# Kernel tuning notes

Hardware: AMD Instinct MI355X
Metric: run time of the kernel (lower is better)

## Reference

```python
import jax, jax.numpy as jnp
import numpy as np

THRESHOLD = 0.5
NEG_POS_RATIO = 3
ALPHA = 1.0
N_CLASSES = 81
B, P, M = 32, 8732, 16


def cxcy_to_xy(c):
    return jnp.concatenate([c[..., :2] - c[..., 2:] / 2, c[..., :2] + c[..., 2:] / 2], -1)


def xy_to_cxcy(x):
    return jnp.concatenate([(x[..., :2] + x[..., 2:]) / 2, x[..., 2:] - x[..., :2]], -1)


def cxcy_to_gcxgcy(c, p):
    # SSD box encoding with variances 0.1 / 0.2
    return jnp.concatenate([(c[..., :2] - p[..., :2]) / (p[..., 2:] / 10.0),
                            jnp.log(c[..., 2:] / p[..., 2:]) * 5.0], -1)


def box_iou(a, b):
    # a: [M,4], b: [P,4] in xy (xmin,ymin,xmax,ymax)
    lt = jnp.maximum(a[:, None, :2], b[None, :, :2])
    rb = jnp.minimum(a[:, None, 2:], b[None, :, 2:])
    wh = jnp.clip(rb - lt, 0.0)
    inter = wh[..., 0] * wh[..., 1]
    area_a = (a[:, 2] - a[:, 0]) * (a[:, 3] - a[:, 1])
    area_b = (b[:, 2] - b[:, 0]) * (b[:, 3] - b[:, 1])
    return inter / (area_a[:, None] + area_b[None, :] - inter)


def setup_inputs() -> dict:
    key = jax.random.key(0)
    k1, k2, k3, k4, k5, k6, k7 = jax.random.split(key, 7)
    predicted_locs = jax.random.normal(k1, (B, P, 4), dtype=jnp.float32)
    predicted_logits = jax.random.normal(k2, (B, P, N_CLASSES), dtype=jnp.float32)
    # valid gt boxes: centers in (0.2,0.8), sizes in (0.05,0.4) -> xy
    cxy = jax.random.uniform(k3, (B, M, 2), minval=0.2, maxval=0.8)
    wh = jax.random.uniform(k4, (B, M, 2), minval=0.05, maxval=0.4)
    boxes = cxcy_to_xy(jnp.concatenate([cxy, wh], -1)).astype(jnp.float32)
    labels = jax.random.randint(k5, (B, M), 1, N_CLASSES)  # real objects: labels >= 1
    # priors: centers in (0,1), positive sizes
    pcxy = jax.random.uniform(k6, (P, 2), minval=0.0, maxval=1.0)
    pwh = jax.random.uniform(k7, (P, 2), minval=0.05, maxval=0.6)
    priors_cxcy = jnp.concatenate([pcxy, pwh], -1).astype(jnp.float32)
    return {"predicted_locs": predicted_locs, "predicted_logits": predicted_logits,
            "boxes": boxes, "labels": labels, "priors_cxcy": priors_cxcy}


def reference(predicted_locs, predicted_logits, boxes, labels, priors_cxcy):
    priors_xy = cxcy_to_xy(priors_cxcy)

    def match(bx, lb):  # bx: [M,4] xy, lb: [M] int
        overlap = box_iou(bx, priors_xy)                # [M, P]
        overlap_for_each_prior = overlap.max(axis=0)    # [P]
        object_for_each_prior = overlap.argmax(axis=0)  # [P]
        prior_for_each_object = overlap.argmax(axis=1)  # [M]
        # force each gt object to be matched to its best prior
        object_for_each_prior = object_for_each_prior.at[prior_for_each_object].set(jnp.arange(M))
        overlap_for_each_prior = overlap_for_each_prior.at[prior_for_each_object].set(1.0)
        label_for_each_prior = lb[object_for_each_prior]
        label_for_each_prior = jnp.where(overlap_for_each_prior < THRESHOLD, 0, label_for_each_prior)
        true_locs = cxcy_to_gcxgcy(xy_to_cxcy(bx[object_for_each_prior]), priors_cxcy)
        return true_locs, label_for_each_prior

    true_locs, true_classes = jax.vmap(match)(boxes, labels)  # [B,P,4], [B,P]

    positive = true_classes != 0                 # [B,P]
    n_positives = positive.sum(axis=1)           # [B]
    n_pos_total = n_positives.sum().astype(jnp.float32)

    # localization: L1Loss (mean) over positive priors only -> mean over 4*n_pos elements
    loc_loss = jnp.sum(jnp.abs(predicted_locs - true_locs) * positive[..., None]) / (4.0 * n_pos_total)

    # per-prior cross entropy, nan/inf -> 0 as in the original
    logp = jax.nn.log_softmax(predicted_logits, axis=-1)
    conf_loss_all = -jnp.take_along_axis(logp, true_classes[..., None], axis=-1)[..., 0]  # [B,P]
    conf_loss_all = jnp.nan_to_num(conf_loss_all, nan=0.0, posinf=0.0, neginf=0.0)

    conf_loss_pos_sum = jnp.sum(conf_loss_all * positive)
    conf_loss_neg = jnp.where(positive, 0.0, conf_loss_all)
    conf_loss_neg = -jnp.sort(-conf_loss_neg, axis=1)  # descending sort per image
    ranks = jnp.arange(P)[None, :]
    hard_negatives = ranks < (NEG_POS_RATIO * n_positives)[:, None]
    conf_loss_hard_neg_sum = jnp.sum(conf_loss_neg * hard_negatives)

    conf_loss = (conf_loss_hard_neg_sum + conf_loss_pos_sum) / n_pos_total
    return conf_loss + ALPHA * loc_loss
```

## Files before the change

### kernel.cpp

```cpp
#include <hip/hip_runtime.h>
#include <math.h>

#define BB 32
#define PP 8732
#define MM 16
#define NC 81
#define THRESH 0.5f
#define NPR 3
#define CHUNKS 16
#define CHUNK ((PP + CHUNKS - 1) / CHUNKS)
#define SBLK 64

__global__ void __launch_bounds__(256) match_part_kernel(
    const float* __restrict__ boxes,
    const float* __restrict__ priors,
    float* __restrict__ ovl,
    int* __restrict__ obj,
    unsigned long long* __restrict__ keys_part)
{
    const int b = blockIdx.x / CHUNKS;
    const int c = blockIdx.x % CHUNKS;
    const int tid = threadIdx.x;
    __shared__ float s_box[MM][4];
    __shared__ float s_area[MM];
    __shared__ float s_bv[4 * MM];
    __shared__ int   s_bi[4 * MM];

    if (tid < MM * 4) ((float*)s_box)[tid] = boxes[b * MM * 4 + tid];
    __syncthreads();
    if (tid < MM)
        s_area[tid] = (s_box[tid][2] - s_box[tid][0]) * (s_box[tid][3] - s_box[tid][1]);
    __syncthreads();

    float bestv[MM];
    int   bestp[MM];
#pragma unroll
    for (int m = 0; m < MM; ++m) { bestv[m] = -1.0f; bestp[m] = 0; }

    const int p0 = c * CHUNK;
    const int p1 = (p0 + CHUNK < PP) ? (p0 + CHUNK) : PP;
    for (int p = p0 + tid; p < p1; p += 256) {
        const float4 pr = ((const float4*)priors)[p];
        float px0 = pr.x - pr.z * 0.5f, py0 = pr.y - pr.w * 0.5f;
        float px1 = pr.x + pr.z * 0.5f, py1 = pr.y + pr.w * 0.5f;
        float parea = (px1 - px0) * (py1 - py0);
        float bv = -1.0f; int bm = 0;
#pragma unroll
        for (int m = 0; m < MM; ++m) {
            float lx = fmaxf(s_box[m][0], px0);
            float ly = fmaxf(s_box[m][1], py0);
            float rx = fminf(s_box[m][2], px1);
            float ry = fminf(s_box[m][3], py1);
            float w = fmaxf(rx - lx, 0.0f);
            float h = fmaxf(ry - ly, 0.0f);
            float inter = w * h;
            float iou = inter / (s_area[m] + parea - inter);
            if (iou > bv) { bv = iou; bm = m; }
            if (iou > bestv[m]) { bestv[m] = iou; bestp[m] = p; }
        }
        ovl[b * PP + p] = bv;
        obj[b * PP + p] = bm;
    }

    const int lane = tid & 63, wid = tid >> 6;
#pragma unroll
    for (int m = 0; m < MM; ++m) {
        float v = bestv[m]; int i = bestp[m];
        for (int off = 32; off > 0; off >>= 1) {
            float ov = __shfl_xor(v, off);
            int   oi = __shfl_xor(i, off);
            if (ov > v || (ov == v && oi < i)) { v = ov; i = oi; }
        }
        if (lane == 0) { s_bv[wid * MM + m] = v; s_bi[wid * MM + m] = i; }
    }
    __syncthreads();

    if (tid == 0) {
        for (int m = 0; m < MM; ++m) {
            float v = s_bv[m]; int i = s_bi[m];
            for (int w = 1; w < 4; ++w) {
                float ov = s_bv[w * MM + m]; int oi = s_bi[w * MM + m];
                if (ov > v || (ov == v && oi < i)) { v = ov; i = oi; }
            }
            if (v < 0.0f) v = 0.0f;
            keys_part[(b * CHUNKS + c) * MM + m] =
                ((unsigned long long)__float_as_uint(v) << 32) |
                (unsigned long long)(0x7FFFFFFFu - (unsigned)i);
        }
    }
}

__global__ void __launch_bounds__(512) force_match_kernel(
    const unsigned long long* __restrict__ keys_part,
    float* __restrict__ ovl, int* __restrict__ obj)
{
    __shared__ int s_p[BB * MM];
    const int tid = threadIdx.x;
    const int b = tid >> 4, m = tid & 15;

    unsigned long long best = 0ull;
#pragma unroll
    for (int c = 0; c < CHUNKS; ++c) {
        unsigned long long k = keys_part[(b * CHUNKS + c) * MM + m];
        if (k > best) best = k;
    }
    s_p[tid] = (int)(0x7FFFFFFFu - (unsigned)(best & 0xFFFFFFFFull));
    __syncthreads();

    if (m == 0) {
        for (int mm = 0; mm < MM; ++mm) {
            int p = s_p[(b << 4) + mm];
            obj[b * PP + p] = mm;
            ovl[b * PP + p] = 1.0f;
        }
    }
}

__global__ void __launch_bounds__(256) conf_kernel(
    const float* __restrict__ logits,
    const float* __restrict__ plocs,
    const float* __restrict__ boxes,
    const int*   __restrict__ labels,
    const float* __restrict__ priors,
    const float* __restrict__ ovl,
    const int*   __restrict__ obj,
    float* __restrict__ neg,
    int*   __restrict__ cnt_part,
    float* __restrict__ conf_part,
    float* __restrict__ loc_part)
{
    const int tid = threadIdx.x;
    const int lane = tid & 63;
    const int g = lane >> 4;
    const int i = lane & 15;
    const int b = blockIdx.x / SBLK;
    const int s = blockIdx.x % SBLK;
    const int w0 = s * 4 + (tid >> 6);
    const int GPI = PP / 4;

    int   pcnt = 0;
    float pconf = 0.0f, ploc = 0.0f;

    for (int wi = w0; wi < GPI; wi += SBLK * 4) {
        const int rp = wi * 4 + g;
        const int r = b * PP + rp;
        const float ov = ovl[r];
        const int o = obj[r];
        const int lab = labels[b * MM + o];

        const size_t base = (size_t)r * NC;
        float e0 = logits[base + i];
        float e1 = logits[base + 16 + i];
        float e2 = logits[base + 32 + i];
        float e3 = logits[base + 48 + i];
        float e4 = logits[base + 64 + i];
        float e5 = (i == 0) ? logits[base + 80] : -INFINITY;

        float mx = fmaxf(fmaxf(fmaxf(e0, e1), fmaxf(e2, e3)), fmaxf(e4, e5));
#pragma unroll
        for (int off = 8; off > 0; off >>= 1) mx = fmaxf(mx, __shfl_xor(mx, off));
        float sum = __expf(e0 - mx) + __expf(e1 - mx) + __expf(e2 - mx) +
                    __expf(e3 - mx) + __expf(e4 - mx) +
                    ((i == 0) ? __expf(e5 - mx) : 0.0f);
#pragma unroll
        for (int off = 8; off > 0; off >>= 1) sum += __shfl_xor(sum, off);

        const int cls = (ov < THRESH) ? 0 : lab;
        const int k = cls >> 4, ci = cls & 15;
        float ek = (k == 0) ? e0 : (k == 1) ? e1 : (k == 2) ? e2 :
                   (k == 3) ? e3 : (k == 4) ? e4 : e5;
        float xc = __shfl(ek, (g << 4) + ci);
        float conf = mx + __logf(sum) - xc;
        if (!isfinite(conf)) conf = 0.0f;

        if (i == 0) {
            neg[r] = (cls == 0) ? conf : 0.0f;
            if (cls != 0) {
                pcnt += 1;
                pconf += conf;
                const float4 bx = ((const float4*)boxes)[b * MM + o];
                float cx = (bx.x + bx.z) * 0.5f;
                float cy = (bx.y + bx.w) * 0.5f;
                float w4 = bx.z - bx.x;
                float h4 = bx.w - bx.y;
                const float4 pr = ((const float4*)priors)[rp];
                float g0 = (cx - pr.x) / (pr.z / 10.0f);
                float g1 = (cy - pr.y) / (pr.w / 10.0f);
                float g2 = logf(w4 / pr.z) * 5.0f;
                float g3 = logf(h4 / pr.w) * 5.0f;
                const float4 pl = ((const float4*)plocs)[r];
                ploc += fabsf(pl.x - g0) + fabsf(pl.y - g1) +
                        fabsf(pl.z - g2) + fabsf(pl.w - g3);
            }
        }
    }

    __shared__ int   s4i[4];
    __shared__ float s4c[4], s4l[4];
#pragma unroll
    for (int off = 32; off > 0; off >>= 1) {
        pcnt  += __shfl_xor(pcnt, off);
        pconf += __shfl_xor(pconf, off);
        ploc  += __shfl_xor(ploc, off);
    }
    const int wv = tid >> 6;
    if (lane == 0) { s4i[wv] = pcnt; s4c[wv] = pconf; s4l[wv] = ploc; }
    __syncthreads();
    if (tid == 0) {
        cnt_part[blockIdx.x]  = s4i[0] + s4i[1] + s4i[2] + s4i[3];
        conf_part[blockIdx.x] = s4c[0] + s4c[1] + s4c[2] + s4c[3];
        loc_part[blockIdx.x]  = s4l[0] + s4l[1] + s4l[2] + s4l[3];
    }
}

#define TPK 1024
#define VPT ((PP + TPK - 1) / TPK)

__global__ void __launch_bounds__(TPK) topk_kernel(
    const float* __restrict__ neg, const int* __restrict__ cnt_part,
    float* __restrict__ hardneg)
{
    const int b = blockIdx.x;
    const int tid = threadIdx.x;
    const int lane = tid & 63, wid = tid >> 6;
    __shared__ int s16i[16];
    __shared__ float s16f[16];
    __shared__ int s_k;

    if (tid < 64) {
        int c = cnt_part[b * SBLK + tid];
#pragma unroll
        for (int off = 32; off > 0; off >>= 1) c += __shfl_xor(c, off);
        if (tid == 0) s_k = NPR * c;
    }

    unsigned v[VPT];
#pragma unroll
    for (int j = 0; j < VPT; ++j) {
        int p = tid + j * TPK;
        v[j] = (p < PP) ? __float_as_uint(neg[b * PP + p]) : 0u;
    }
    __syncthreads();

    int K = s_k;
    if (K > PP) K = PP;
    if (K <= 0) { if (tid == 0) hardneg[b] = 0.0f; return; }

    unsigned lo = 0u, hi = 0x7fffffffu;
    while (lo < hi) {
        unsigned mid = lo + ((hi - lo + 1u) >> 1);
        int cnt = 0;
#pragma unroll
        for (int j = 0; j < VPT; ++j) cnt += (v[j] >= mid);
#pragma unroll
        for (int off = 32; off > 0; off >>= 1) cnt += __shfl_xor(cnt, off);
        if (lane == 0) s16i[wid] = cnt;
        __syncthreads();
        int total = 0;
#pragma unroll
        for (int j = 0; j < 16; ++j) total += s16i[j];
        __syncthreads();
        if (total >= K) lo = mid; else hi = mid - 1u;
    }
    const unsigned kth = lo;

    int cgt = 0; float sgt = 0.0f;
#pragma unroll
    for (int j = 0; j < VPT; ++j) {
        if (v[j] > kth) { cgt++; sgt += __uint_as_float(v[j]); }
    }
#pragma unroll
    for (int off = 32; off > 0; off >>= 1) {
        cgt += __shfl_xor(cgt, off);
        sgt += __shfl_xor(sgt, off);
    }
    if (lane == 0) { s16i[wid] = cgt; s16f[wid] = sgt; }
    __syncthreads();
    if (tid == 0) {
        int cgt_t = 0; float sum_gt = 0.0f;
#pragma unroll
        for (int j = 0; j < 16; ++j) { cgt_t += s16i[j]; sum_gt += s16f[j]; }
        hardneg[b] = sum_gt + (float)(K - cgt_t) * __uint_as_float(kth);
    }
}

__global__ void __launch_bounds__(256) final_kernel(
    const int* __restrict__ cnt_part,
    const float* __restrict__ conf_part,
    const float* __restrict__ loc_part,
    const float* __restrict__ hardneg,
    float* __restrict__ out)
{
    const int tid = threadIdx.x;
    const int lane = tid & 63, wid = tid >> 6;
    __shared__ int s4i[4];
    __shared__ float s4c[4], s4l[4], s4h[4];

    int np = 0; float cf = 0.0f, lc = 0.0f, hn = 0.0f;
    for (int j = tid; j < BB * SBLK; j += 256) {
        np += cnt_part[j];
        cf += conf_part[j];
        lc += loc_part[j];
    }
    if (tid < BB) hn = hardneg[tid];

#pragma unroll
    for (int off = 32; off > 0; off >>= 1) {
        np += __shfl_xor(np, off);
        cf += __shfl_xor(cf, off);
        lc += __shfl_xor(lc, off);
        hn += __shfl_xor(hn, off);
    }
    if (lane == 0) { s4i[wid] = np; s4c[wid] = cf; s4l[wid] = lc; s4h[wid] = hn; }
    __syncthreads();
    if (tid == 0) {
        float npt = (float)(s4i[0] + s4i[1] + s4i[2] + s4i[3]);
        float cft = s4c[0] + s4c[1] + s4c[2] + s4c[3];
        float lct = s4l[0] + s4l[1] + s4l[2] + s4l[3];
        float hnt = s4h[0] + s4h[1] + s4h[2] + s4h[3];
        out[0] = (hnt + cft) / npt + lct / (4.0f * npt);
    }
}

extern "C" void kernel_launch(void* const* d_in, const int* in_sizes, int n_in,
                              void* d_out, int out_size, void* d_ws, size_t ws_size,
                              hipStream_t stream) {
    (void)in_sizes; (void)n_in; (void)out_size; (void)ws_size;
    const float* plocs  = (const float*)d_in[0];
    const float* logits = (const float*)d_in[1];
    const float* boxes  = (const float*)d_in[2];
    const int*   labels = (const int*)d_in[3];
    const float* priors = (const float*)d_in[4];
    float* out = (float*)d_out;

    char* ws = (char*)d_ws;
    float* ovl      = (float*)ws; ws += (size_t)BB * PP * 4;
    int*   obj      = (int*)ws;   ws += (size_t)BB * PP * 4;
    float* neg      = (float*)ws; ws += (size_t)BB * PP * 4;
    unsigned long long* keys_part = (unsigned long long*)ws; ws += (size_t)BB * CHUNKS * MM * 8;
    int*   cnt_part  = (int*)ws;   ws += BB * SBLK * 4;
    float* conf_part = (float*)ws; ws += BB * SBLK * 4;
    float* loc_part  = (float*)ws; ws += BB * SBLK * 4;
    float* hardneg   = (float*)ws; ws += BB * 4;


    match_part_kernel<<<BB * CHUNKS, 256, 0, stream>>>(boxes, priors, ovl, obj, keys_part);
    force_match_kernel<<<1, 512, 0, stream>>>(keys_part, ovl, obj);

    conf_kernel<<<BB * SBLK, 256, 0, stream>>>(logits, plocs, boxes, labels, priors,
                                               ovl, obj, neg,
                                               cnt_part, conf_part, loc_part);

    topk_kernel<<<BB, TPK, 0, stream>>>(neg, cnt_part, hardneg);

    final_kernel<<<1, 256, 0, stream>>>(cnt_part, conf_part, loc_part, hardneg, out);
}
```

Baseline: 75.23 us.

## Recompute per-prior IoU in conf kernel and fuse force-match and final reduction

The match kernel no longer writes per-prior best overlap and object index. It only produces the per-object best-prior keys. The conf kernel recomputes the IoU per prior, with one lane per gt box, takes the argmax with shuffles, and applies the forced matches through a ballot over the reduced keys. The separate force-match and final kernels are removed: the last top-k block, found with an atomic counter, does the global reduction. This cuts two launches and the ovl/obj global round trips, at the cost of redundant IoU math and a fence-based last-block pattern.

Measured after the change: 87.43 us. +16.2%, slower.

```diff
diff --git a/kernel.cpp b/kernel.cpp
--- a/kernel.cpp
+++ b/kernel.cpp
@@ -14,13 +14,14 @@
 __global__ void __launch_bounds__(256) match_part_kernel(
     const float* __restrict__ boxes,
     const float* __restrict__ priors,
-    float* __restrict__ ovl,
-    int* __restrict__ obj,
-    unsigned long long* __restrict__ keys_part)
+    unsigned long long* __restrict__ keys_part,
+    unsigned* __restrict__ done)
 {
     const int b = blockIdx.x / CHUNKS;
     const int c = blockIdx.x % CHUNKS;
     const int tid = threadIdx.x;
+    if (blockIdx.x == 0 && tid == 0) *done = 0u;
+
     __shared__ float s_box[MM][4];
     __shared__ float s_area[MM];
     __shared__ float s_bv[4 * MM];
@@ -44,7 +45,6 @@
         float px0 = pr.x - pr.z * 0.5f, py0 = pr.y - pr.w * 0.5f;
         float px1 = pr.x + pr.z * 0.5f, py1 = pr.y + pr.w * 0.5f;
         float parea = (px1 - px0) * (py1 - py0);
-        float bv = -1.0f; int bm = 0;
 #pragma unroll
         for (int m = 0; m < MM; ++m) {
             float lx = fmaxf(s_box[m][0], px0);
@@ -55,11 +55,8 @@
             float h = fmaxf(ry - ly, 0.0f);
             float inter = w * h;
             float iou = inter / (s_area[m] + parea - inter);
-            if (iou > bv) { bv = iou; bm = m; }
             if (iou > bestv[m]) { bestv[m] = iou; bestp[m] = p; }
         }
-        ovl[b * PP + p] = bv;
-        obj[b * PP + p] = bm;
     }
 
     const int lane = tid & 63, wid = tid >> 6;
@@ -90,40 +87,13 @@
     }
 }
 
-__global__ void __launch_bounds__(512) force_match_kernel(
-    const unsigned long long* __restrict__ keys_part,
-    float* __restrict__ ovl, int* __restrict__ obj)
-{
-    __shared__ int s_p[BB * MM];
-    const int tid = threadIdx.x;
-    const int b = tid >> 4, m = tid & 15;
-
-    unsigned long long best = 0ull;
-#pragma unroll
-    for (int c = 0; c < CHUNKS; ++c) {
-        unsigned long long k = keys_part[(b * CHUNKS + c) * MM + m];
-        if (k > best) best = k;
-    }
-    s_p[tid] = (int)(0x7FFFFFFFu - (unsigned)(best & 0xFFFFFFFFull));
-    __syncthreads();
-
-    if (m == 0) {
-        for (int mm = 0; mm < MM; ++mm) {
-            int p = s_p[(b << 4) + mm];
-            obj[b * PP + p] = mm;
-            ovl[b * PP + p] = 1.0f;
-        }
-    }
-}
-
 __global__ void __launch_bounds__(256) conf_kernel(
     const float* __restrict__ logits,
     const float* __restrict__ plocs,
     const float* __restrict__ boxes,
     const int*   __restrict__ labels,
     const float* __restrict__ priors,
-    const float* __restrict__ ovl,
-    const int*   __restrict__ obj,
+    const unsigned long long* __restrict__ keys_part,
     float* __restrict__ neg,
     int*   __restrict__ cnt_part,
     float* __restrict__ conf_part,
@@ -135,6 +105,34 @@
     const int i = lane & 15;
     const int b = blockIdx.x / SBLK;
     const int s = blockIdx.x % SBLK;
+
+    __shared__ float s_box[MM][4];
+    __shared__ float s_area[MM];
+    __shared__ int   s_lab[MM];
+    __shared__ int   s_fp[MM];
+    __shared__ unsigned long long s_keys[CHUNKS * MM];
+
+    if (tid < MM * 4) ((float*)s_box)[tid] = boxes[b * MM * 4 + tid];
+    if (tid < MM) s_lab[tid] = labels[b * MM + tid];
+    s_keys[tid] = keys_part[b * CHUNKS * MM + tid];
+    __syncthreads();
+    if (tid < MM) {
+        s_area[tid] = (s_box[tid][2] - s_box[tid][0]) * (s_box[tid][3] - s_box[tid][1]);
+        unsigned long long best = 0ull;
+#pragma unroll
+        for (int c = 0; c < CHUNKS; ++c) {
+            unsigned long long k = s_keys[c * MM + tid];
+            if (k > best) best = k;
+        }
+        s_fp[tid] = (int)(0x7FFFFFFFu - (unsigned)(best & 0xFFFFFFFFull));
+    }
+    __syncthreads();
+
+    const float bxx0 = s_box[i][0], bxy0 = s_box[i][1];
+    const float bxx1 = s_box[i][2], bxy1 = s_box[i][3];
+    const float barea = s_area[i];
+    const int   myfp  = s_fp[i];
+
     const int w0 = s * 4 + (tid >> 6);
     const int GPI = PP / 4;
 
@@ -144,9 +142,27 @@
     for (int wi = w0; wi < GPI; wi += SBLK * 4) {
         const int rp = wi * 4 + g;
         const int r = b * PP + rp;
-        const float ov = ovl[r];
-        const int o = obj[r];
-        const int lab = labels[b * MM + o];
+
+        const float4 pr = ((const float4*)priors)[rp];
+        float px0 = pr.x - pr.z * 0.5f, py0 = pr.y - pr.w * 0.5f;
+        float px1 = pr.x + pr.z * 0.5f, py1 = pr.y + pr.w * 0.5f;
+        float parea = (px1 - px0) * (py1 - py0);
+        float lx = fmaxf(bxx0, px0), ly = fmaxf(bxy0, py0);
+        float rx = fminf(bxx1, px1), ry = fminf(bxy1, py1);
+        float inter = fmaxf(rx - lx, 0.0f) * fmaxf(ry - ly, 0.0f);
+        float ov = inter / (barea + parea - inter);
+        int bm = i;
+#pragma unroll
+        for (int off = 8; off > 0; off >>= 1) {
+            float o2 = __shfl_xor(ov, off);
+            int   i2 = __shfl_xor(bm, off);
+            if (o2 > ov || (o2 == ov && i2 < bm)) { ov = o2; bm = i2; }
+        }
+        unsigned long long bal = __ballot(myfp == rp);
+        unsigned gm = (unsigned)((bal >> (g * 16)) & 0xFFFFull);
+        int o, cls;
+        if (gm) { o = 31 - __clz(gm); cls = s_lab[o]; }
+        else    { o = bm; cls = (ov < THRESH) ? 0 : s_lab[bm]; }
 
         const size_t base = (size_t)r * NC;
         float e0 = logits[base + i];
@@ -165,7 +181,6 @@
 #pragma unroll
         for (int off = 8; off > 0; off >>= 1) sum += __shfl_xor(sum, off);
 
-        const int cls = (ov < THRESH) ? 0 : lab;
         const int k = cls >> 4, ci = cls & 15;
         float ek = (k == 0) ? e0 : (k == 1) ? e1 : (k == 2) ? e2 :
                    (k == 3) ? e3 : (k == 4) ? e4 : e5;
@@ -178,12 +193,10 @@
             if (cls != 0) {
                 pcnt += 1;
                 pconf += conf;
-                const float4 bx = ((const float4*)boxes)[b * MM + o];
-                float cx = (bx.x + bx.z) * 0.5f;
-                float cy = (bx.y + bx.w) * 0.5f;
-                float w4 = bx.z - bx.x;
-                float h4 = bx.w - bx.y;
-                const float4 pr = ((const float4*)priors)[rp];
+                float cx = (s_box[o][0] + s_box[o][2]) * 0.5f;
+                float cy = (s_box[o][1] + s_box[o][3]) * 0.5f;
+                float w4 = s_box[o][2] - s_box[o][0];
+                float h4 = s_box[o][3] - s_box[o][1];
                 float g0 = (cx - pr.x) / (pr.z / 10.0f);
                 float g1 = (cy - pr.y) / (pr.w / 10.0f);
                 float g2 = logf(w4 / pr.z) * 5.0f;
@@ -216,9 +229,11 @@
 #define TPK 1024
 #define VPT ((PP + TPK - 1) / TPK)
 
-__global__ void __launch_bounds__(TPK) topk_kernel(
+__global__ void __launch_bounds__(TPK) topk_final_kernel(
     const float* __restrict__ neg, const int* __restrict__ cnt_part,
-    float* __restrict__ hardneg)
+    const float* __restrict__ conf_part, const float* __restrict__ loc_part,
+    float* __restrict__ hardneg, unsigned* __restrict__ done,
+    float* __restrict__ out)
 {
     const int b = blockIdx.x;
     const int tid = threadIdx.x;
@@ -226,6 +241,7 @@
     __shared__ int s16i[16];
     __shared__ float s16f[16];
     __shared__ int s_k;
+    __shared__ int s_last;
 
     if (tid < 64) {
         int c = cnt_part[b * SBLK + tid];
@@ -244,66 +260,63 @@
 
     int K = s_k;
     if (K > PP) K = PP;
-    if (K <= 0) { if (tid == 0) hardneg[b] = 0.0f; return; }
-
-    unsigned lo = 0u, hi = 0x7fffffffu;
-    while (lo < hi) {
-        unsigned mid = lo + ((hi - lo + 1u) >> 1);
-        int cnt = 0;
-#pragma unroll
-        for (int j = 0; j < VPT; ++j) cnt += (v[j] >= mid);
-#pragma unroll
-        for (int off = 32; off > 0; off >>= 1) cnt += __shfl_xor(cnt, off);
-        if (lane == 0) s16i[wid] = cnt;
+    if (K > 0) {
+        unsigned lo = 0u, hi = 0x7fffffffu;
+        while (lo < hi) {
+            unsigned mid = lo + ((hi - lo + 1u) >> 1);
+            int cnt = 0;
+#pragma unroll
+            for (int j = 0; j < VPT; ++j) cnt += (v[j] >= mid);
+#pragma unroll
+            for (int off = 32; off > 0; off >>= 1) cnt += __shfl_xor(cnt, off);
+            if (lane == 0) s16i[wid] = cnt;
+            __syncthreads();
+            int total = 0;
+#pragma unroll
+            for (int j = 0; j < 16; ++j) total += s16i[j];
+            __syncthreads();
+            if (total >= K) lo = mid; else hi = mid - 1u;
+        }
+        const unsigned kth = lo;
+
+        int cgt = 0; float sgt = 0.0f;
+#pragma unroll
+        for (int j = 0; j < VPT; ++j) {
+            if (v[j] > kth) { cgt++; sgt += __uint_as_float(v[j]); }
+        }
+#pragma unroll
+        for (int off = 32; off > 0; off >>= 1) {
+            cgt += __shfl_xor(cgt, off);
+            sgt += __shfl_xor(sgt, off);
+        }
+        if (lane == 0) { s16i[wid] = cgt; s16f[wid] = sgt; }
         __syncthreads();
-        int total = 0;
-#pragma unroll
-        for (int j = 0; j < 16; ++j) total += s16i[j];
-        __syncthreads();
-        if (total >= K) lo = mid; else hi = mid - 1u;
-    }
-    const unsigned kth = lo;
-
-    int cgt = 0; float sgt = 0.0f;
-#pragma unroll
-    for (int j = 0; j < VPT; ++j) {
-        if (v[j] > kth) { cgt++; sgt += __uint_as_float(v[j]); }
-    }
-#pragma unroll
-    for (int off = 32; off > 0; off >>= 1) {
-        cgt += __shfl_xor(cgt, off);
-        sgt += __shfl_xor(sgt, off);
-    }
-    if (lane == 0) { s16i[wid] = cgt; s16f[wid] = sgt; }
-    __syncthreads();
+        if (tid == 0) {
+            int cgt_t = 0; float sum_gt = 0.0f;
+#pragma unroll
+            for (int j = 0; j < 16; ++j) { cgt_t += s16i[j]; sum_gt += s16f[j]; }
+            hardneg[b] = sum_gt + (float)(K - cgt_t) * __uint_as_float(kth);
+        }
+    } else {
+        if (tid == 0) hardneg[b] = 0.0f;
+    }
+
+    __threadfence();
     if (tid == 0) {
-        int cgt_t = 0; float sum_gt = 0.0f;
-#pragma unroll
-        for (int j = 0; j < 16; ++j) { cgt_t += s16i[j]; sum_gt += s16f[j]; }
-        hardneg[b] = sum_gt + (float)(K - cgt_t) * __uint_as_float(kth);
-    }
-}
-
-__global__ void __launch_bounds__(256) final_kernel(
-    const int* __restrict__ cnt_part,
-    const float* __restrict__ conf_part,
-    const float* __restrict__ loc_part,
-    const float* __restrict__ hardneg,
-    float* __restrict__ out)
-{
-    const int tid = threadIdx.x;
-    const int lane = tid & 63, wid = tid >> 6;
-    __shared__ int s4i[4];
-    __shared__ float s4c[4], s4l[4], s4h[4];
+        unsigned old = atomicAdd(done, 1u);
+        s_last = (old == BB - 1) ? 1 : 0;
+    }
+    __syncthreads();
+    if (!s_last) return;
+    __threadfence();
 
     int np = 0; float cf = 0.0f, lc = 0.0f, hn = 0.0f;
-    for (int j = tid; j < BB * SBLK; j += 256) {
+    for (int j = tid; j < BB * SBLK; j += TPK) {
         np += cnt_part[j];
         cf += conf_part[j];
         lc += loc_part[j];
     }
     if (tid < BB) hn = hardneg[tid];
-
 #pragma unroll
     for (int off = 32; off > 0; off >>= 1) {
         np += __shfl_xor(np, off);
@@ -311,13 +324,17 @@
         lc += __shfl_xor(lc, off);
         hn += __shfl_xor(hn, off);
     }
-    if (lane == 0) { s4i[wid] = np; s4c[wid] = cf; s4l[wid] = lc; s4h[wid] = hn; }
+    if (lane == 0) { s16i[wid] = np; s16f[wid] = cf; }
+    __shared__ float s16l[16], s16h[16];
+    if (lane == 0) { s16l[wid] = lc; s16h[wid] = hn; }
     __syncthreads();
     if (tid == 0) {
-        float npt = (float)(s4i[0] + s4i[1] + s4i[2] + s4i[3]);
-        float cft = s4c[0] + s4c[1] + s4c[2] + s4c[3];
-        float lct = s4l[0] + s4l[1] + s4l[2] + s4l[3];
-        float hnt = s4h[0] + s4h[1] + s4h[2] + s4h[3];
+        int npt_i = 0; float cft = 0.0f, lct = 0.0f, hnt = 0.0f;
+#pragma unroll
+        for (int j = 0; j < 16; ++j) {
+            npt_i += s16i[j]; cft += s16f[j]; lct += s16l[j]; hnt += s16h[j];
+        }
+        float npt = (float)npt_i;
         out[0] = (hnt + cft) / npt + lct / (4.0f * npt);
     }
 }
@@ -334,24 +351,21 @@
     float* out = (float*)d_out;
 
     char* ws = (char*)d_ws;
-    float* ovl      = (float*)ws; ws += (size_t)BB * PP * 4;
-    int*   obj      = (int*)ws;   ws += (size_t)BB * PP * 4;
     float* neg      = (float*)ws; ws += (size_t)BB * PP * 4;
     unsigned long long* keys_part = (unsigned long long*)ws; ws += (size_t)BB * CHUNKS * MM * 8;
     int*   cnt_part  = (int*)ws;   ws += BB * SBLK * 4;
     float* conf_part = (float*)ws; ws += BB * SBLK * 4;
     float* loc_part  = (float*)ws; ws += BB * SBLK * 4;
     float* hardneg   = (float*)ws; ws += BB * 4;
-
-
-    match_part_kernel<<<BB * CHUNKS, 256, 0, stream>>>(boxes, priors, ovl, obj, keys_part);
-    force_match_kernel<<<1, 512, 0, stream>>>(keys_part, ovl, obj);
+    unsigned* done   = (unsigned*)ws; ws += 4;
+
+
+    match_part_kernel<<<BB * CHUNKS, 256, 0, stream>>>(boxes, priors, keys_part, done);
 
     conf_kernel<<<BB * SBLK, 256, 0, stream>>>(logits, plocs, boxes, labels, priors,
-                                               ovl, obj, neg,
+                                               keys_part, neg,
                                                cnt_part, conf_part, loc_part);
 
-    topk_kernel<<<BB, TPK, 0, stream>>>(neg, cnt_part, hardneg);
-
-    final_kernel<<<1, 256, 0, stream>>>(cnt_part, conf_part, loc_part, hardneg, out);
+    topk_final_kernel<<<BB, TPK, 0, stream>>>(neg, cnt_part, conf_part, loc_part,
+                                              hardneg, done, out);
 }
```
